# Kernel optimization log

Hardware: AMD Instinct MI355X
Metric: run time of the kernel (lower is better)

Reference implementation:

```python
import jax, jax.numpy as jnp
import numpy as np

NB, NLOC, DIN, DOUT = 4, 4096, 512, 512
NTYPES, TEBD = 128, 128
N_EXPERTS, TOP_K = 8, 2  # share_expert = 0 -> routed_experts = 8, routed_top_k = 2


def setup_inputs() -> dict:
    key = jax.random.key(0)
    k = jax.random.split(key, 6)
    return {
        "x": jax.random.normal(k[0], (NB, NLOC, DIN), dtype=jnp.float32),
        "type_embeddings": jax.random.normal(k[1], (NTYPES, TEBD), dtype=jnp.float32),
        "atom_types": jax.random.randint(k[2], (NB, NLOC), 0, NTYPES, dtype=jnp.int32),
        "Wg": jax.random.normal(k[3], (TEBD, N_EXPERTS), dtype=jnp.float32) / np.sqrt(TEBD),
        "We": jax.random.normal(k[4], (N_EXPERTS, DIN, DOUT), dtype=jnp.float32) / np.sqrt(DIN),
        "be": jax.random.normal(k[5], (N_EXPERTS, DOUT), dtype=jnp.float32) * 0.01,
    }


def reference(x, type_embeddings, atom_types, Wg, We, be):
    # --- route: gate on type embeddings, then index per atom (MD-continuous) ---
    logits = type_embeddings @ Wg                       # [ntypes, E]
    top_vals, top_idx = jax.lax.top_k(logits, TOP_K)    # [ntypes, K]
    weights = jax.nn.softmax(top_vals, axis=-1)         # softmax over selected logits
    atom_w = weights[atom_types]                        # [nb, nloc, K]
    atom_i = top_idx[atom_types]                        # [nb, nloc, K]

    # scatter-add top-k weights into dense per-expert weights (matches scatter_add_)
    onehot = jax.nn.one_hot(atom_i, N_EXPERTS, dtype=x.dtype)   # [nb, nloc, K, E]
    per_expert_w = jnp.einsum("bnk,bnke->bne", atom_w, onehot)  # [nb, nloc, E]

    # --- run all experts densely (the batched JIT-friendly path), then combine ---
    expert_out = jnp.tanh(jnp.einsum("bnd,edo->bneo", x, We) + be)  # [nb, nloc, E, dout]
    out = jnp.einsum("bne,bneo->bno", per_expert_w, expert_out)     # [nb, nloc, dout]
    return out
```

## Files before the change

kernel.cpp:

```cpp
#include <hip/hip_runtime.h>
#include <hip/hip_bf16.h>
#include <math.h>

typedef __bf16 bf16;
typedef __bf16 bf16x8 __attribute__((ext_vector_type(8)));
typedef float  f32x4  __attribute__((ext_vector_type(4)));

#define NTOK   16384
#define DIN    512
#define DOUT   512
#define NTYPES 128
#define TEBD   128
#define NEXP   8
#define NPAIR  64
#define MAXTILE 192

#define WS_HIST    0
#define WS_ROUTE_W 512
#define WS_BASET   1536
#define WS_CURS    2048
#define WS_CNTP    2560
#define WS_BASEP   2816
#define WS_NTILE   3072
#define WS_TMAP    3584
#define WS_RMAP    5120
#define WS_WGT     (WS_RMAP + NTOK * 4)
#define WS_XG      (WS_WGT + NTOK * 8)
#define WS_WET     (WS_XG + (size_t)NTOK * DIN * 2)

#define GLOAD_LDS16(g, l)                                                     \
  __builtin_amdgcn_global_load_lds(                                           \
      (const __attribute__((address_space(1))) void*)(g),                     \
      (__attribute__((address_space(3))) void*)(l), 16, 0, 0)

__global__ void hist_kernel(const int* __restrict__ atype, int* __restrict__ hist) {
  __shared__ int h[NTYPES];
  int tid = threadIdx.x;
  if (tid < NTYPES) h[tid] = 0;
  __syncthreads();
  int t = blockIdx.x * 256 + tid;
  atomicAdd(&h[atype[t]], 1);
  __syncthreads();
  if (tid < NTYPES && h[tid]) atomicAdd(&hist[tid], h[tid]);
}

__global__ void route_scan_kernel(const float* __restrict__ emb,
                                  const float* __restrict__ Wg,
                                  const int* __restrict__ hist,
                                  float* __restrict__ route_w,
                                  int* __restrict__ base_type,
                                  int* __restrict__ cursor,
                                  int* __restrict__ cnt_pair,
                                  int* __restrict__ base_pair,
                                  int* __restrict__ ntile,
                                  int* __restrict__ tmap) {
  __shared__ int s_cnt[NPAIR];
  __shared__ int s_off[NTYPES];
  __shared__ int s_pair[NTYPES];
  int t = threadIdx.x;
  if (t < NPAIR) s_cnt[t] = 0;
  __syncthreads();

  const float* er = emb + (size_t)t * TEBD;
  float lg[NEXP];
#pragma unroll
  for (int e = 0; e < NEXP; ++e) lg[e] = 0.f;
  for (int j = 0; j < TEBD; ++j) {
    float ev = er[j];
#pragma unroll
    for (int e = 0; e < NEXP; ++e) lg[e] += ev * Wg[j * NEXP + e];
  }
  float v0 = -__builtin_inff(), v1 = -__builtin_inff();
  int i0 = 0, i1 = 0;
#pragma unroll
  for (int e = 0; e < NEXP; ++e) {
    float v = lg[e];
    if (v > v0) { v1 = v0; i1 = i0; v0 = v; i0 = e; }
    else if (v > v1) { v1 = v; i1 = e; }
  }
  float d = expf(v1 - v0);
  float inv = 1.f / (1.f + d);
  route_w[t * 2 + 0] = inv;
  route_w[t * 2 + 1] = d * inv;
  int p = i0 * 8 + i1;
  s_pair[t] = p;
  s_off[t] = atomicAdd(&s_cnt[p], hist[t]);
  cursor[t] = 0;
  __syncthreads();

  if (t < NPAIR) {
    int b = 0, tb = 0;
    for (int j = 0; j < t; ++j) { b += s_cnt[j]; tb += (s_cnt[j] + 127) >> 7; }
    base_pair[t] = b;
    cnt_pair[t] = s_cnt[t];
    int nt_l = (s_cnt[t] + 127) >> 7;
    for (int i = 0; i < nt_l; ++i) {
      tmap[(tb + i) * 2 + 0] = t;
      tmap[(tb + i) * 2 + 1] = i * 128;
    }
    if (t == NPAIR - 1) ntile[0] = tb + nt_l;
  }
  __syncthreads();
  base_type[t] = base_pair[s_pair[t]] + s_off[t];
}

__global__ void prep_kernel(const float* __restrict__ x,
                            const float* __restrict__ We,
                            const int* __restrict__ atype,
                            const float* __restrict__ route_w,
                            const int* __restrict__ base_type,
                            int* __restrict__ cursor,
                            int* __restrict__ row_map,
                            float* __restrict__ wgt,
                            bf16* __restrict__ xg,
                            bf16* __restrict__ WeT) {
  int bx = blockIdx.x;
  int tid = threadIdx.x;
  if (bx < 256) {
    __shared__ int posS[64];
    int t0 = bx * 64;
    if (tid < 64) {
      int t = t0 + tid;
      int ty = atype[t];
      int pos = base_type[ty] + atomicAdd(&cursor[ty], 1);
      posS[tid] = pos;
      row_map[pos] = t;
      ((float2*)wgt)[pos] = ((const float2*)route_w)[ty];
    }
    __syncthreads();
    int w = tid >> 6, lane = tid & 63;
#pragma unroll
    for (int i = 0; i < 16; ++i) {
      int r = w * 16 + i;
      const float4* p = (const float4*)(x + (size_t)(t0 + r) * DIN + lane * 8);
      float4 a = p[0], b = p[1];
      bf16x8 o;
      o[0] = (bf16)a.x; o[1] = (bf16)a.y; o[2] = (bf16)a.z; o[3] = (bf16)a.w;
      o[4] = (bf16)b.x; o[5] = (bf16)b.y; o[6] = (bf16)b.z; o[7] = (bf16)b.w;
      *(bf16x8*)(xg + (size_t)posS[r] * DIN + lane * 8) = o;
    }
  } else {
    __shared__ float t[64][65];
    int b2 = bx - 256;
    int e = b2 >> 6;
    int rem = b2 & 63;
    int kt = (rem >> 3) * 64;
    int nt = (rem & 7) * 64;
    int col = tid & 63;
    int rq = tid >> 6;
#pragma unroll
    for (int r = 0; r < 16; ++r) {
      int row = rq * 16 + r;
      t[row][col] = We[((size_t)e * DIN + kt + row) * DOUT + nt + col];
    }
    __syncthreads();
#pragma unroll
    for (int r = 0; r < 16; ++r) {
      int n = rq * 16 + r;
      WeT[((size_t)e * DOUT + nt + n) * DIN + kt + col] = (bf16)t[col][n];
    }
  }
}

__global__ __launch_bounds__(256, 3) void moe_gemm_pair_kernel(
    const bf16* __restrict__ xg, const bf16* __restrict__ WeT,
    const float* __restrict__ be, const int* __restrict__ cnt_pair,
    const int* __restrict__ base_pair, const int* __restrict__ ntile,
    const int* __restrict__ tmap, const int* __restrict__ row_map,
    const float* __restrict__ wgt, float* __restrict__ out) {
  int nwork = ntile[0] * 8;
  int f = blockIdx.y * 8 + blockIdx.x;
  if (f >= nwork) return;
  int q = nwork >> 3, r = nwork & 7;
  int xcd = f & 7, idx = f >> 3;
  int L = (xcd < r ? xcd * (q + 1) : r * (q + 1) + (xcd - r) * q) + idx;
  int ti = L >> 3;
  int cx = L & 7;
  int list = tmap[ti * 2 + 0];
  int r0   = tmap[ti * 2 + 1];
  int e0 = list >> 3, e1 = list & 7;
  int nrow = cnt_pair[list] - r0;
  if (nrow > 128) nrow = 128;
  int c0 = cx * 64;
  int arow0 = base_pair[list] + r0;

  __shared__ __align__(16) bf16 As[3][128 * 32];
  __shared__ __align__(16) bf16 B0s[3][64 * 32];
  __shared__ __align__(16) bf16 B1s[3][64 * 32];
  __shared__ int   tokS[128];
  __shared__ float w0S[128], w1S[128];
  __shared__ float be0S[64], be1S[64];

  int tid = threadIdx.x;
  int lane = tid & 63, w = tid >> 6;

  if (tid < 128) {
    int srow = (tid < nrow) ? tid : (nrow - 1);
    int gl = arow0 + srow;
    tokS[tid] = row_map[gl];
    float2 ww = ((const float2*)wgt)[gl];
    w0S[tid] = ww.x;
    w1S[tid] = ww.y;
    if (tid < 64) {
      be0S[tid] = be[e0 * DOUT + c0 + tid];
      be1S[tid] = be[e1 * DOUT + c0 + tid];
    }
  }
  __syncthreads();

  const bf16* srcA[2];
#pragma unroll
  for (int j = 0; j < 2; ++j) {
    int slot = w * 128 + j * 64 + lane;
    int row = slot >> 2, cs = slot & 3;
    int c = cs ^ ((row >> 1) & 3);
    int srow = (row < nrow) ? row : (nrow - 1);
    srcA[j] = xg + (size_t)(arow0 + srow) * DIN + c * 8;
  }
  const bf16* srcB0;
  const bf16* srcB1;
  {
    int slot = w * 64 + lane;
    int row = slot >> 2, cs = slot & 3;
    int c = cs ^ ((row >> 1) & 3);
    srcB0 = WeT + ((size_t)e0 * DOUT + c0 + row) * DIN + c * 8;
    srcB1 = WeT + ((size_t)e1 * DOUT + c0 + row) * DIN + c * 8;
  }

  f32x4 acc0[4][2], acc1[4][2];
#pragma unroll
  for (int mi = 0; mi < 4; ++mi)
#pragma unroll
    for (int ni = 0; ni < 2; ++ni) { acc0[mi][ni] = (f32x4)0.f; acc1[mi][ni] = (f32x4)0.f; }

  int wm = (w >> 1) * 64;
  int wn = (w & 1) * 32;
  int r16 = lane & 15, g16 = lane >> 4;

  int offA[4], offB[2];
#pragma unroll
  for (int i = 0; i < 4; ++i) {
    int rA = wm + i * 16 + r16;
    offA[i] = rA * 32 + (g16 ^ ((rA >> 1) & 3)) * 8;
  }
#pragma unroll
  for (int i = 0; i < 2; ++i) {
    int rB = wn + i * 16 + r16;
    offB[i] = rB * 32 + (g16 ^ ((rB >> 1) & 3)) * 8;
  }

  auto stage = [&](int buf) {
#pragma unroll
    for (int j = 0; j < 2; ++j) {
      GLOAD_LDS16(srcA[j], &As[buf][(w * 128 + j * 64) * 8]);
      srcA[j] += 32;
    }
    GLOAD_LDS16(srcB0, &B0s[buf][w * 64 * 8]);
    GLOAD_LDS16(srcB1, &B1s[buf][w * 64 * 8]);
    srcB0 += 32;
    srcB1 += 32;
  };

  stage(0);
  stage(1);

#pragma unroll
  for (int t = 0; t < 16; ++t) {
    if (t < 15) asm volatile("s_waitcnt vmcnt(4)" ::: "memory");
    else        asm volatile("s_waitcnt vmcnt(0)" ::: "memory");
    __builtin_amdgcn_s_barrier();
    if (t + 2 < 16) stage((t + 2) % 3);

    int cur = t % 3;
    bf16x8 af[4], b0f[2], b1f[2];
#pragma unroll
    for (int i = 0; i < 4; ++i) af[i] = *(const bf16x8*)&As[cur][offA[i]];
#pragma unroll
    for (int i = 0; i < 2; ++i) b0f[i] = *(const bf16x8*)&B0s[cur][offB[i]];
#pragma unroll
    for (int i = 0; i < 2; ++i) b1f[i] = *(const bf16x8*)&B1s[cur][offB[i]];
    __builtin_amdgcn_s_setprio(1);
#pragma unroll
    for (int mi = 0; mi < 4; ++mi)
#pragma unroll
      for (int ni = 0; ni < 2; ++ni) {
        acc0[mi][ni] = __builtin_amdgcn_mfma_f32_16x16x32_bf16(
            af[mi], b0f[ni], acc0[mi][ni], 0, 0, 0);
        acc1[mi][ni] = __builtin_amdgcn_mfma_f32_16x16x32_bf16(
            af[mi], b1f[ni], acc1[mi][ni], 0, 0, 0);
      }
    __builtin_amdgcn_s_setprio(0);
  }

#pragma unroll
  for (int mi = 0; mi < 4; ++mi) {
#pragma unroll
    for (int ni = 0; ni < 2; ++ni) {
      f32x4 v0 = acc0[mi][ni];
      f32x4 v1 = acc1[mi][ni];
      int colLocal = wn + ni * 16 + r16;
      float bev0 = be0S[colLocal];
      float bev1 = be1S[colLocal];
#pragma unroll
      for (int r = 0; r < 4; ++r) {
        int lrow = wm + mi * 16 + g16 * 4 + r;
        if (lrow < nrow) {
          float x0 = fminf(9.f, fmaxf(-9.f, v0[r] + bev0)) * 2.885390082f;
          float x1 = fminf(9.f, fmaxf(-9.f, v1[r] + bev1)) * 2.885390082f;
          float e0v, e1v, invd;
          asm("v_exp_f32 %0, %1" : "=v"(e0v) : "v"(x0));
          asm("v_exp_f32 %0, %1" : "=v"(e1v) : "v"(x1));
          float d0 = e0v + 1.f, d1 = e1v + 1.f;
          asm("v_rcp_f32 %0, %1" : "=v"(invd) : "v"(d0 * d1));
          float t0 = (e0v - 1.f) * d1 * invd;
          float t1 = (e1v - 1.f) * d0 * invd;
          out[(size_t)tokS[lrow] * DOUT + c0 + colLocal] =
              t0 * w0S[lrow] + t1 * w1S[lrow];
        }
      }
    }
  }
}

extern "C" void kernel_launch(void* const* d_in, const int* in_sizes, int n_in,
                              void* d_out, int out_size, void* d_ws, size_t ws_size,
                              hipStream_t stream) {
  const float* x    = (const float*)d_in[0];
  const float* emb  = (const float*)d_in[1];
  const int*   aty  = (const int*)d_in[2];
  const float* Wg   = (const float*)d_in[3];
  const float* We   = (const float*)d_in[4];
  const float* be   = (const float*)d_in[5];
  float* out = (float*)d_out;

  char* ws = (char*)d_ws;
  int*   hist      = (int*)(ws + WS_HIST);
  float* route_w   = (float*)(ws + WS_ROUTE_W);
  int*   base_type = (int*)(ws + WS_BASET);
  int*   cursor    = (int*)(ws + WS_CURS);
  int*   cnt_pair  = (int*)(ws + WS_CNTP);
  int*   base_pair = (int*)(ws + WS_BASEP);
  int*   ntile     = (int*)(ws + WS_NTILE);
  int*   tmap      = (int*)(ws + WS_TMAP);
  int*   row_map   = (int*)(ws + WS_RMAP);
  float* wgt       = (float*)(ws + WS_WGT);
  bf16*  xg        = (bf16*)(ws + WS_XG);
  bf16*  WeT       = (bf16*)(ws + WS_WET);

  hipMemsetAsync(hist, 0, NTYPES * sizeof(int), stream);
  hist_kernel<<<NTOK / 256, 256, 0, stream>>>(aty, hist);
  route_scan_kernel<<<1, 128, 0, stream>>>(emb, Wg, hist, route_w, base_type,
                                           cursor, cnt_pair, base_pair, ntile, tmap);
  prep_kernel<<<256 + 512, 256, 0, stream>>>(x, We, aty, route_w, base_type,
                                             cursor, row_map, wgt, xg, WeT);
  moe_gemm_pair_kernel<<<dim3(8, MAXTILE), 256, 0, stream>>>(
      xg, WeT, be, cnt_pair, base_pair, ntile, tmap, row_map, wgt, out);
}
```

Before: 77.87 us.

## Enlarge MoE GEMM tiles to 256x128 with 512 threads and drop histogram memset

The grouped pair GEMM now uses 256-row by 128-column tiles with 8 waves per block, each wave holding a 64x64 sub-tile for both experts. The goal is more reuse of each staged A and B tile and fewer blocks. The histogram kernel writes per-block partial counts that the routing kernel sums, so the memset launch and global atomics are gone. Per-tile metadata loads are now issued after the first prefetch stages so they overlap with them. In exchange, larger tiles mean more padded rows in the last tile of each expert pair, fewer blocks to spread across CUs, and higher register pressure.

```diff
diff --git a/kernel.cpp b/kernel.cpp
--- a/kernel.cpp
+++ b/kernel.cpp
@@ -13,17 +13,19 @@
 #define TEBD   128
 #define NEXP   8
 #define NPAIR  64
-#define MAXTILE 192
-
-#define WS_HIST    0
-#define WS_ROUTE_W 512
-#define WS_BASET   1536
-#define WS_CURS    2048
-#define WS_CNTP    2560
-#define WS_BASEP   2816
-#define WS_NTILE   3072
-#define WS_TMAP    3584
-#define WS_RMAP    5120
+#define BM     256
+#define BNE    128
+#define MAXT   128
+
+#define WS_HPART   0
+#define WS_ROUTE_W 32768
+#define WS_BASET   33792
+#define WS_CURS    34304
+#define WS_CNTP    34816
+#define WS_BASEP   35072
+#define WS_NTILE   35328
+#define WS_TMAP    35840
+#define WS_RMAP    36864
 #define WS_WGT     (WS_RMAP + NTOK * 4)
 #define WS_XG      (WS_WGT + NTOK * 8)
 #define WS_WET     (WS_XG + (size_t)NTOK * DIN * 2)
@@ -33,7 +35,7 @@
       (const __attribute__((address_space(1))) void*)(g),                     \
       (__attribute__((address_space(3))) void*)(l), 16, 0, 0)
 
-__global__ void hist_kernel(const int* __restrict__ atype, int* __restrict__ hist) {
+__global__ void hist_kernel(const int* __restrict__ atype, int* __restrict__ hpart) {
   __shared__ int h[NTYPES];
   int tid = threadIdx.x;
   if (tid < NTYPES) h[tid] = 0;
@@ -41,12 +43,12 @@
   int t = blockIdx.x * 256 + tid;
   atomicAdd(&h[atype[t]], 1);
   __syncthreads();
-  if (tid < NTYPES && h[tid]) atomicAdd(&hist[tid], h[tid]);
+  if (tid < NTYPES) hpart[blockIdx.x * NTYPES + tid] = h[tid];
 }
 
 __global__ void route_scan_kernel(const float* __restrict__ emb,
                                   const float* __restrict__ Wg,
-                                  const int* __restrict__ hist,
+                                  const int* __restrict__ hpart,
                                   float* __restrict__ route_w,
                                   int* __restrict__ base_type,
                                   int* __restrict__ cursor,
@@ -61,6 +63,9 @@
   if (t < NPAIR) s_cnt[t] = 0;
   __syncthreads();
 
+  int myc = 0;
+  for (int b = 0; b < 64; ++b) myc += hpart[b * NTYPES + t];
+
   const float* er = emb + (size_t)t * TEBD;
   float lg[NEXP];
 #pragma unroll
@@ -84,19 +89,19 @@
   route_w[t * 2 + 1] = d * inv;
   int p = i0 * 8 + i1;
   s_pair[t] = p;
-  s_off[t] = atomicAdd(&s_cnt[p], hist[t]);
+  s_off[t] = atomicAdd(&s_cnt[p], myc);
   cursor[t] = 0;
   __syncthreads();
 
   if (t < NPAIR) {
     int b = 0, tb = 0;
-    for (int j = 0; j < t; ++j) { b += s_cnt[j]; tb += (s_cnt[j] + 127) >> 7; }
+    for (int j = 0; j < t; ++j) { b += s_cnt[j]; tb += (s_cnt[j] + BM - 1) >> 8; }
     base_pair[t] = b;
     cnt_pair[t] = s_cnt[t];
-    int nt_l = (s_cnt[t] + 127) >> 7;
+    int nt_l = (s_cnt[t] + BM - 1) >> 8;
     for (int i = 0; i < nt_l; ++i) {
       tmap[(tb + i) * 2 + 0] = t;
-      tmap[(tb + i) * 2 + 1] = i * 128;
+      tmap[(tb + i) * 2 + 1] = i * BM;
     }
     if (t == NPAIR - 1) ntile[0] = tb + nt_l;
   }
@@ -162,51 +167,37 @@
   }
 }
 
-__global__ __launch_bounds__(256, 3) void moe_gemm_pair_kernel(
+__global__ __launch_bounds__(512, 2) void moe_gemm_pair_kernel(
     const bf16* __restrict__ xg, const bf16* __restrict__ WeT,
     const float* __restrict__ be, const int* __restrict__ cnt_pair,
     const int* __restrict__ base_pair, const int* __restrict__ ntile,
     const int* __restrict__ tmap, const int* __restrict__ row_map,
     const float* __restrict__ wgt, float* __restrict__ out) {
-  int nwork = ntile[0] * 8;
-  int f = blockIdx.y * 8 + blockIdx.x;
+  int nwork = ntile[0] * 4;
+  int f = blockIdx.y * 4 + blockIdx.x;
   if (f >= nwork) return;
   int q = nwork >> 3, r = nwork & 7;
   int xcd = f & 7, idx = f >> 3;
   int L = (xcd < r ? xcd * (q + 1) : r * (q + 1) + (xcd - r) * q) + idx;
-  int ti = L >> 3;
-  int cx = L & 7;
+  int ti = L >> 2;
+  int cx = L & 3;
   int list = tmap[ti * 2 + 0];
   int r0   = tmap[ti * 2 + 1];
   int e0 = list >> 3, e1 = list & 7;
   int nrow = cnt_pair[list] - r0;
-  if (nrow > 128) nrow = 128;
-  int c0 = cx * 64;
+  if (nrow > BM) nrow = BM;
+  int c0 = cx * BNE;
   int arow0 = base_pair[list] + r0;
 
-  __shared__ __align__(16) bf16 As[3][128 * 32];
-  __shared__ __align__(16) bf16 B0s[3][64 * 32];
-  __shared__ __align__(16) bf16 B1s[3][64 * 32];
-  __shared__ int   tokS[128];
-  __shared__ float w0S[128], w1S[128];
-  __shared__ float be0S[64], be1S[64];
+  __shared__ __align__(16) bf16 As[3][BM * 32];
+  __shared__ __align__(16) bf16 B0s[3][BNE * 32];
+  __shared__ __align__(16) bf16 B1s[3][BNE * 32];
+  __shared__ int   tokS[BM];
+  __shared__ float w0S[BM], w1S[BM];
+  __shared__ float be0S[BNE], be1S[BNE];
 
   int tid = threadIdx.x;
   int lane = tid & 63, w = tid >> 6;
-
-  if (tid < 128) {
-    int srow = (tid < nrow) ? tid : (nrow - 1);
-    int gl = arow0 + srow;
-    tokS[tid] = row_map[gl];
-    float2 ww = ((const float2*)wgt)[gl];
-    w0S[tid] = ww.x;
-    w1S[tid] = ww.y;
-    if (tid < 64) {
-      be0S[tid] = be[e0 * DOUT + c0 + tid];
-      be1S[tid] = be[e1 * DOUT + c0 + tid];
-    }
-  }
-  __syncthreads();
 
   const bf16* srcA[2];
 #pragma unroll
@@ -227,28 +218,6 @@
     srcB1 = WeT + ((size_t)e1 * DOUT + c0 + row) * DIN + c * 8;
   }
 
-  f32x4 acc0[4][2], acc1[4][2];
-#pragma unroll
-  for (int mi = 0; mi < 4; ++mi)
-#pragma unroll
-    for (int ni = 0; ni < 2; ++ni) { acc0[mi][ni] = (f32x4)0.f; acc1[mi][ni] = (f32x4)0.f; }
-
-  int wm = (w >> 1) * 64;
-  int wn = (w & 1) * 32;
-  int r16 = lane & 15, g16 = lane >> 4;
-
-  int offA[4], offB[2];
-#pragma unroll
-  for (int i = 0; i < 4; ++i) {
-    int rA = wm + i * 16 + r16;
-    offA[i] = rA * 32 + (g16 ^ ((rA >> 1) & 3)) * 8;
-  }
-#pragma unroll
-  for (int i = 0; i < 2; ++i) {
-    int rB = wn + i * 16 + r16;
-    offB[i] = rB * 32 + (g16 ^ ((rB >> 1) & 3)) * 8;
-  }
-
   auto stage = [&](int buf) {
 #pragma unroll
     for (int j = 0; j < 2; ++j) {
@@ -264,6 +233,38 @@
   stage(0);
   stage(1);
 
+  if (tid < BM) {
+    int srow = (tid < nrow) ? tid : (nrow - 1);
+    int gl = arow0 + srow;
+    tokS[tid] = row_map[gl];
+    float2 ww = ((const float2*)wgt)[gl];
+    w0S[tid] = ww.x;
+    w1S[tid] = ww.y;
+    if (tid < BNE) {
+      be0S[tid] = be[e0 * DOUT + c0 + tid];
+      be1S[tid] = be[e1 * DOUT + c0 + tid];
+    }
+  }
+
+  f32x4 acc0[4][4], acc1[4][4];
+#pragma unroll
+  for (int mi = 0; mi < 4; ++mi)
+#pragma unroll
+    for (int ni = 0; ni < 4; ++ni) { acc0[mi][ni] = (f32x4)0.f; acc1[mi][ni] = (f32x4)0.f; }
+
+  int wmi = w >> 1;
+  int wni = w & 1;
+  int r16 = lane & 15, g16 = lane >> 4;
+
+  int offA[4], offB[4];
+#pragma unroll
+  for (int i = 0; i < 4; ++i) {
+    int rA = wmi * 64 + i * 16 + r16;
+    offA[i] = rA * 32 + (g16 ^ ((rA >> 1) & 3)) * 8;
+    int rB = wni * 64 + i * 16 + r16;
+    offB[i] = rB * 32 + (g16 ^ ((rB >> 1) & 3)) * 8;
+  }
+
 #pragma unroll
   for (int t = 0; t < 16; ++t) {
     if (t < 15) asm volatile("s_waitcnt vmcnt(4)" ::: "memory");
@@ -272,18 +273,18 @@
     if (t + 2 < 16) stage((t + 2) % 3);
 
     int cur = t % 3;
-    bf16x8 af[4], b0f[2], b1f[2];
+    bf16x8 af[4], b0f[4], b1f[4];
 #pragma unroll
     for (int i = 0; i < 4; ++i) af[i] = *(const bf16x8*)&As[cur][offA[i]];
 #pragma unroll
-    for (int i = 0; i < 2; ++i) b0f[i] = *(const bf16x8*)&B0s[cur][offB[i]];
-#pragma unroll
-    for (int i = 0; i < 2; ++i) b1f[i] = *(const bf16x8*)&B1s[cur][offB[i]];
+    for (int i = 0; i < 4; ++i) b0f[i] = *(const bf16x8*)&B0s[cur][offB[i]];
+#pragma unroll
+    for (int i = 0; i < 4; ++i) b1f[i] = *(const bf16x8*)&B1s[cur][offB[i]];
     __builtin_amdgcn_s_setprio(1);
 #pragma unroll
     for (int mi = 0; mi < 4; ++mi)
 #pragma unroll
-      for (int ni = 0; ni < 2; ++ni) {
+      for (int ni = 0; ni < 4; ++ni) {
         acc0[mi][ni] = __builtin_amdgcn_mfma_f32_16x16x32_bf16(
             af[mi], b0f[ni], acc0[mi][ni], 0, 0, 0);
         acc1[mi][ni] = __builtin_amdgcn_mfma_f32_16x16x32_bf16(
@@ -295,15 +296,15 @@
 #pragma unroll
   for (int mi = 0; mi < 4; ++mi) {
 #pragma unroll
-    for (int ni = 0; ni < 2; ++ni) {
+    for (int ni = 0; ni < 4; ++ni) {
       f32x4 v0 = acc0[mi][ni];
       f32x4 v1 = acc1[mi][ni];
-      int colLocal = wn + ni * 16 + r16;
+      int colLocal = wni * 64 + ni * 16 + r16;
       float bev0 = be0S[colLocal];
       float bev1 = be1S[colLocal];
 #pragma unroll
       for (int r = 0; r < 4; ++r) {
-        int lrow = wm + mi * 16 + g16 * 4 + r;
+        int lrow = wmi * 64 + mi * 16 + g16 * 4 + r;
         if (lrow < nrow) {
           float x0 = fminf(9.f, fmaxf(-9.f, v0[r] + bev0)) * 2.885390082f;
           float x1 = fminf(9.f, fmaxf(-9.f, v1[r] + bev1)) * 2.885390082f;
@@ -334,7 +335,7 @@
   float* out = (float*)d_out;
 
   char* ws = (char*)d_ws;
-  int*   hist      = (int*)(ws + WS_HIST);
+  int*   hpart     = (int*)(ws + WS_HPART);
   float* route_w   = (float*)(ws + WS_ROUTE_W);
   int*   base_type = (int*)(ws + WS_BASET);
   int*   cursor    = (int*)(ws + WS_CURS);
@@ -347,12 +348,11 @@
   bf16*  xg        = (bf16*)(ws + WS_XG);
   bf16*  WeT       = (bf16*)(ws + WS_WET);
 
-  hipMemsetAsync(hist, 0, NTYPES * sizeof(int), stream);
-  hist_kernel<<<NTOK / 256, 256, 0, stream>>>(aty, hist);
-  route_scan_kernel<<<1, 128, 0, stream>>>(emb, Wg, hist, route_w, base_type,
+  hist_kernel<<<NTOK / 256, 256, 0, stream>>>(aty, hpart);
+  route_scan_kernel<<<1, 128, 0, stream>>>(emb, Wg, hpart, route_w, base_type,
                                            cursor, cnt_pair, base_pair, ntile, tmap);
   prep_kernel<<<256 + 512, 256, 0, stream>>>(x, We, aty, route_w, base_type,
                                              cursor, row_map, wgt, xg, WeT);
-  moe_gemm_pair_kernel<<<dim3(8, MAXTILE), 256, 0, stream>>>(
+  moe_gemm_pair_kernel<<<dim3(4, MAXT), 512, 0, stream>>>(
       xg, WeT, be, cnt_pair, base_pair, ntile, tmap, row_map, wgt, out);
 }
```

After: 88.37 us. 1.13x slower.
